# Optimization experiments

Hardware: AMD Instinct MI355X
Metric: run time of the kernel (lower is better)

Reference implementation:

```python
import jax, jax.numpy as jnp
import numpy as np

D_MODEL = 1024
N_HEAD = 16
D_K = D_MODEL // N_HEAD


def setup_inputs() -> dict:
    key = jax.random.key(0)
    ks = jax.random.split(key, 11)
    B, S = 2, 2048
    scale = 1.0 / np.sqrt(D_MODEL)
    inp = {
        "q": jax.random.normal(ks[0], (B, S, D_MODEL), jnp.float32),
        "k": jax.random.normal(ks[1], (B, S, D_MODEL), jnp.float32),
        "v": jax.random.normal(ks[2], (B, S, D_MODEL), jnp.float32),
        "Wq": jax.random.normal(ks[3], (D_MODEL, D_MODEL), jnp.float32) * scale,
        "bq": jnp.zeros((D_MODEL,), jnp.float32),
        "Wk": jax.random.normal(ks[4], (D_MODEL, D_MODEL), jnp.float32) * scale,
        "bk": jnp.zeros((D_MODEL,), jnp.float32),
        "Wv": jax.random.normal(ks[5], (D_MODEL, D_MODEL), jnp.float32) * scale,
        "bv": jnp.zeros((D_MODEL,), jnp.float32),
        "Wo": jax.random.normal(ks[6], (D_MODEL, D_MODEL), jnp.float32) * scale,
        "bo": jnp.zeros((D_MODEL,), jnp.float32),
    }
    return inp


def _split_heads(x):
    B, S, _ = x.shape
    return x.reshape(B, S, N_HEAD, D_K).transpose(0, 2, 1, 3)  # [B,H,S,Dk]


def reference(q, k, v, Wq, bq, Wk, bk, Wv, bv, Wo, bo):
    # Linear projections (torch Linear: x @ W.T + b)
    qh = _split_heads(q @ Wq.T + bq)
    kh = _split_heads(k @ Wk.T + bk)
    vh = _split_heads(v @ Wv.T + bv)
    # naive scaled dot-product attention, full [B,H,S,S] scores
    score = jnp.einsum("bhqd,bhkd->bhqk", qh, kh) / jnp.sqrt(jnp.float32(D_K))
    attn = jax.nn.softmax(score, axis=-1)
    out = jnp.einsum("bhqk,bhkd->bhqd", attn, vh)
    B, H, S, Dk = out.shape
    out = out.transpose(0, 2, 1, 3).reshape(B, S, H * Dk)
    return out @ Wo.T + bo
```

## Files before the change

kernel.cpp:

```cpp
#include <hip/hip_runtime.h>

typedef __attribute__((ext_vector_type(8))) short bh8;
typedef __attribute__((ext_vector_type(4))) float fx4;
typedef __attribute__((ext_vector_type(16))) float fx16;
typedef __attribute__((ext_vector_type(4))) unsigned short us4;
typedef unsigned short u16;

__device__ __forceinline__ u16 f2bf(float x) {
  unsigned u = __float_as_uint(x);
  u += 0x7fffu + ((u >> 16) & 1u);
  return (u16)(u >> 16);
}

__device__ __forceinline__ void async16(const void* g, void* l) {
  __builtin_amdgcn_global_load_lds(
      (const __attribute__((address_space(1))) void*)g,
      (__attribute__((address_space(3))) void*)l,
      16, 0, 0);
}

__global__ __launch_bounds__(256) void k_convert(
    const float* __restrict__ q, const float* __restrict__ k, const float* __restrict__ v,
    const float* __restrict__ wq, const float* __restrict__ wk,
    const float* __restrict__ wv, const float* __restrict__ wo,
    u16* __restrict__ dst) {
  size_t gid = (size_t)blockIdx.x * 256 + threadIdx.x;
  size_t e4 = gid * 4;
  const float* src; size_t off;
  if (e4 < 4194304)        { src = q;  off = e4; }
  else if (e4 < 8388608)   { src = k;  off = e4 - 4194304; }
  else if (e4 < 12582912)  { src = v;  off = e4 - 8388608; }
  else if (e4 < 13631488)  { src = wq; off = e4 - 12582912; }
  else if (e4 < 14680064)  { src = wk; off = e4 - 13631488; }
  else if (e4 < 15728640)  { src = wv; off = e4 - 14680064; }
  else                     { src = wo; off = e4 - 15728640; }
  float4 f = *(const float4*)(src + off);
  us4 o; o.x = f2bf(f.x); o.y = f2bf(f.y); o.z = f2bf(f.z); o.w = f2bf(f.w);
  *(us4*)(dst + e4) = o;
}

template<int BM>
__device__ __forceinline__ void gemm_stageT(const u16* __restrict__ A, const u16* __restrict__ B,
                                            char* lds, int bufbase, int m0, int n0, int kt, int tid) {
  int wb16 = (tid & 0xC0) * 16;
  #pragma unroll
  for (int i = 0; i < BM / 64; ++i) {
    int cl = i * 256 + tid;
    int row = cl >> 2, ch = cl & 3;
    int sch = ch ^ (row & 3);
    const char* ga = (const char*)(A + (size_t)(m0 + row) * 1024 + kt * 32) + sch * 16;
    async16(ga, lds + bufbase + i * 4096 + wb16);
  }
  #pragma unroll
  for (int i = 0; i < 2; ++i) {
    int cl = i * 256 + tid;
    int row = cl >> 2, ch = cl & 3;
    int sch = ch ^ (row & 3);
    const char* gb = (const char*)(B + (size_t)(n0 + row) * 1024 + kt * 32) + sch * 16;
    async16(gb, lds + bufbase + BM * 64 + i * 4096 + wb16);
  }
}

template<int BM>
__device__ __forceinline__ void gemm_coreT(const u16* __restrict__ A, const u16* __restrict__ Bw,
                                           const float* __restrict__ bias, void* Cout, int mode,
                                           float scl, char* lds) {
  constexpr int MF = BM / 32;
  constexpr int BUFSZ = BM * 64 + 8192;
  int tid = threadIdx.x;
  int lane = tid & 63, w = tid >> 6, g = lane >> 4, cc = lane & 15;
  int wr = w >> 1, wc = w & 1;
  int m0 = blockIdx.y * BM, n0 = blockIdx.x * 128;
  fx4 acc[MF][4] = {};
  gemm_stageT<BM>(A, Bw, lds, 0, m0, n0, 0, tid);
  for (int kt = 0; kt < 32; ++kt) {
    __syncthreads();
    if (kt + 1 < 32) gemm_stageT<BM>(A, Bw, lds, ((kt + 1) & 1) * BUFSZ, m0, n0, kt + 1, tid);
    const char* bA = lds + (kt & 1) * BUFSZ;
    const char* bB = bA + BM * 64;
    bh8 af[MF], bf[4];
    #pragma unroll
    for (int mf = 0; mf < MF; ++mf) {
      int row = wr * (BM / 2) + mf * 16 + cc;
      af[mf] = *(const bh8*)(bA + row * 64 + ((g ^ (row & 3)) * 16));
    }
    #pragma unroll
    for (int nf = 0; nf < 4; ++nf) {
      int row = wc * 64 + nf * 16 + cc;
      bf[nf] = *(const bh8*)(bB + row * 64 + ((g ^ (row & 3)) * 16));
    }
    #pragma unroll
    for (int mf = 0; mf < MF; ++mf)
      #pragma unroll
      for (int nf = 0; nf < 4; ++nf)
        acc[mf][nf] = __builtin_amdgcn_mfma_f32_16x16x32_bf16(af[mf], bf[nf], acc[mf][nf], 0, 0, 0);
  }
  #pragma unroll
  for (int mf = 0; mf < MF; ++mf) {
    #pragma unroll
    for (int nf = 0; nf < 4; ++nf) {
      fx4 a = acc[mf][nf];
      int row = m0 + wr * (BM / 2) + mf * 16 + g * 4;
      int col = n0 + wc * 64 + nf * 16 + cc;
      float bv = bias[col];
      if (mode == 0) {
        u16* C = (u16*)Cout;
        #pragma unroll
        for (int r = 0; r < 4; ++r) C[(size_t)(row + r) * 1024 + col] = f2bf((a[r] + bv) * scl);
      } else if (mode == 1) {
        float* C = (float*)Cout;
        #pragma unroll
        for (int r = 0; r < 4; ++r) C[(size_t)(row + r) * 1024 + col] = (a[r] + bv) * scl;
      } else {
        u16* C = (u16*)Cout;
        us4 o;
        #pragma unroll
        for (int r = 0; r < 4; ++r) o[r] = f2bf((a[r] + bv) * scl);
        int bb = row >> 11;
        *(us4*)(C + (size_t)(bb * 1024 + col) * 2048 + (row & 2047)) = o;
      }
    }
  }
}

__global__ __launch_bounds__(256) void k_gemm_qkv(
    const u16* __restrict__ qb, const u16* __restrict__ kb, const u16* __restrict__ vb,
    const u16* __restrict__ wqb, const u16* __restrict__ wkb, const u16* __restrict__ wvb,
    const float* __restrict__ bq, const float* __restrict__ bk, const float* __restrict__ bv,
    u16* __restrict__ Qp, u16* __restrict__ Kp, u16* __restrict__ Vt) {
  __shared__ __align__(16) char lds[32768];
  int z = blockIdx.z;
  const u16* A = (z == 0) ? qb : (z == 1) ? kb : vb;
  const u16* B = (z == 0) ? wqb : (z == 1) ? wkb : wvb;
  const float* bias = (z == 0) ? bq : (z == 1) ? bk : bv;
  void* C = (z == 0) ? (void*)Qp : (z == 1) ? (void*)Kp : (void*)Vt;
  float scl = (z == 0) ? 0.18033688f : 1.0f;
  gemm_coreT<128>(A, B, bias, C, (z == 2) ? 2 : 0, scl, lds);
}

__global__ __launch_bounds__(256) void k_gemm_out(
    const u16* __restrict__ Ob, const u16* __restrict__ wob,
    const float* __restrict__ bo, float* __restrict__ out) {
  __shared__ __align__(16) char lds[24576];
  gemm_coreT<64>(Ob, wob, bo, out, 1, 1.0f, lds);
}

__global__ __launch_bounds__(256) void k_attn(
    const u16* __restrict__ Qp, const u16* __restrict__ Kp,
    const u16* __restrict__ Vt, u16* __restrict__ O) {
  __shared__ __align__(16) char lds[65536];
  int tid = threadIdx.x;
  int lane = tid & 63, w = tid >> 6, ql = lane & 31, hi = lane >> 5;
  int lin = blockIdx.y * 16 + blockIdx.x;
  int xcd = lin & 7, slot = lin >> 3;
  int bh = xcd * 4 + (slot >> 4), qtile = slot & 15;
  int b = bh >> 4, h = bh & 15;
  int q0 = qtile * 128 + w * 32;
  size_t qrow = (size_t)b * 2048 + q0 + ql;
  bh8 qf[4];
  #pragma unroll
  for (int ds = 0; ds < 4; ++ds)
    qf[ds] = *(const bh8*)(Qp + qrow * 1024 + h * 64 + ds * 16 + hi * 8);

  int r0 = tid >> 3;
  int gr0 = (r0 & 19) | (((r0 >> 2) & 1) << 3) | (((r0 >> 3) & 1) << 2);
  int sK = (tid & 7) ^ (r0 & 7);
  const char* gK = (const char*)(Kp + (size_t)(b * 2048 + gr0) * 1024 + h * 64) + sK * 16;
  int vr0 = tid >> 4;
  int sV = (tid & 15) ^ (vr0 & 7);
  const char* gV = (const char*)(Vt + ((size_t)(b * 1024 + h * 64 + vr0)) * 2048) + sV * 16;
  int wb16 = (tid & 0xC0) * 16;

  int x7 = ql & 7;
  int kbase = ql * 128, vbase = ql * 256;
  int kc[4], vc[8];
  #pragma unroll
  for (int ds = 0; ds < 4; ++ds) kc[ds] = ((ds * 2 + hi) ^ x7) * 16;
  #pragma unroll
  for (int ks = 0; ks < 8; ++ks) vc[ks] = ((ks * 2 + hi) ^ x7) * 16;

  float lpart = 0.f;
  fx16 ot[2] = {};
  #pragma unroll
  for (int i = 0; i < 4; ++i) {
    async16(gK + i * 65536, lds + i * 4096 + wb16);
    async16(gV + i * 65536, lds + 16384 + i * 4096 + wb16);
  }
  gK += 262144; gV += 256;

  for (int t = 0; t < 16; ++t) {
    __syncthreads();
    if (t + 1 < 16) {
      int bb = ((t + 1) & 1) << 15;
      #pragma unroll
      for (int i = 0; i < 4; ++i) {
        async16(gK + i * 65536, lds + bb + i * 4096 + wb16);
        async16(gV + i * 65536, lds + bb + 16384 + i * 4096 + wb16);
      }
      gK += 262144; gV += 256;
    }
    const char* bK = lds + ((t & 1) << 15);
    const char* bV = bK + 16384;
    fx16 st[4] = {};
    #pragma unroll
    for (int kk = 0; kk < 4; ++kk)
      #pragma unroll
      for (int ds = 0; ds < 4; ++ds)
        st[kk] = __builtin_amdgcn_mfma_f32_32x32x16_bf16(
            *(const bh8*)(bK + kk * 4096 + kbase + kc[ds]), qf[ds], st[kk], 0, 0, 0);
    bh8 Pf[8];
    #pragma unroll
    for (int kk = 0; kk < 4; ++kk) {
      #pragma unroll
      for (int m = 0; m < 2; ++m) {
        float p[8];
        #pragma unroll
        for (int e = 0; e < 8; ++e) p[e] = __builtin_amdgcn_exp2f(st[kk][8 * m + e]);
        lpart += ((p[0] + p[1]) + (p[2] + p[3])) + ((p[4] + p[5]) + (p[6] + p[7]));
        unsigned u0, u1, u2, u3;
        asm("v_cvt_pk_bf16_f32 %0, %1, %2" : "=v"(u0) : "v"(p[0]), "v"(p[1]));
        asm("v_cvt_pk_bf16_f32 %0, %1, %2" : "=v"(u1) : "v"(p[2]), "v"(p[3]));
        asm("v_cvt_pk_bf16_f32 %0, %1, %2" : "=v"(u2) : "v"(p[4]), "v"(p[5]));
        asm("v_cvt_pk_bf16_f32 %0, %1, %2" : "=v"(u3) : "v"(p[6]), "v"(p[7]));
        union { unsigned u[4]; bh8 v; } pu;
        pu.u[0] = u0; pu.u[1] = u1; pu.u[2] = u2; pu.u[3] = u3;
        Pf[kk * 2 + m] = pu.v;
      }
    }
    #pragma unroll
    for (int dt = 0; dt < 2; ++dt)
      #pragma unroll
      for (int ks = 0; ks < 8; ++ks)
        ot[dt] = __builtin_amdgcn_mfma_f32_32x32x16_bf16(
            *(const bh8*)(bV + dt * 8192 + vbase + vc[ks]), Pf[ks], ot[dt], 0, 0, 0);
  }
  float lsum = lpart + __shfl_xor(lpart, 32);
  float inv = 1.f / lsum;
  #pragma unroll
  for (int dt = 0; dt < 2; ++dt)
    #pragma unroll
    for (int j = 0; j < 4; ++j) {
      us4 o4;
      #pragma unroll
      for (int i = 0; i < 4; ++i) o4[i] = f2bf(ot[dt][4 * j + i] * inv);
      *(us4*)(O + qrow * 1024 + h * 64 + dt * 32 + j * 8 + hi * 4) = o4;
    }
}

extern "C" void kernel_launch(void* const* d_in, const int* in_sizes, int n_in,
                              void* d_out, int out_size, void* d_ws, size_t ws_size,
                              hipStream_t stream) {
  const float* q  = (const float*)d_in[0];
  const float* k  = (const float*)d_in[1];
  const float* v  = (const float*)d_in[2];
  const float* Wq = (const float*)d_in[3];
  const float* bq = (const float*)d_in[4];
  const float* Wk = (const float*)d_in[5];
  const float* bk = (const float*)d_in[6];
  const float* Wv = (const float*)d_in[7];
  const float* bv = (const float*)d_in[8];
  const float* Wo = (const float*)d_in[9];
  const float* bo = (const float*)d_in[10];
  u16* ws  = (u16*)d_ws;
  u16* qb  = ws;
  u16* kb  = qb + 4194304;
  u16* vb  = kb + 4194304;
  u16* wqb = vb + 4194304;
  u16* wkb = wqb + 1048576;
  u16* wvb = wkb + 1048576;
  u16* wob = wvb + 1048576;
  u16* Qp  = wob + 1048576;
  u16* Kp  = Qp + 4194304;
  u16* Vt  = Kp + 4194304;
  u16* Ob  = qb;

  k_convert<<<dim3(16384), 256, 0, stream>>>(q, k, v, Wq, Wk, Wv, Wo, qb);
  k_gemm_qkv<<<dim3(8, 32, 3), 256, 0, stream>>>(qb, kb, vb, wqb, wkb, wvb, bq, bk, bv, Qp, Kp, Vt);
  k_attn<<<dim3(16, 32), 256, 0, stream>>>(Qp, Kp, Vt, Ob);
  k_gemm_out<<<dim3(8, 64), 256, 0, stream>>>(Ob, wob, bo, (float*)d_out);
}
```

Measured before the change: 122.8 us.

## Fuse fp32-to-bf16 activation conversion into QKV GEMM A-tile staging

The separate conversion pass over q, k and v is removed; the QKV GEMM now loads fp32 activation tiles into registers, converts them with packed bf16 conversion instructions and writes them into swizzled LDS. The register loads for the next tile are issued before the MFMA loop and stored after it, to overlap them with compute. This avoids writing and re-reading 24M bf16 activation elements, at the cost of reading fp32 A from global memory once per N-tile column (eight times) and moving A staging off the async global-to-LDS path. The rounding mode may differ slightly from the previous manual round-to-nearest-even.

```diff
diff --git a/kernel.cpp b/kernel.cpp
--- a/kernel.cpp
+++ b/kernel.cpp
@@ -20,28 +20,38 @@
 }
 
 __global__ __launch_bounds__(256) void k_convert(
-    const float* __restrict__ q, const float* __restrict__ k, const float* __restrict__ v,
     const float* __restrict__ wq, const float* __restrict__ wk,
     const float* __restrict__ wv, const float* __restrict__ wo,
     u16* __restrict__ dst) {
   size_t gid = (size_t)blockIdx.x * 256 + threadIdx.x;
   size_t e4 = gid * 4;
   const float* src; size_t off;
-  if (e4 < 4194304)        { src = q;  off = e4; }
-  else if (e4 < 8388608)   { src = k;  off = e4 - 4194304; }
-  else if (e4 < 12582912)  { src = v;  off = e4 - 8388608; }
-  else if (e4 < 13631488)  { src = wq; off = e4 - 12582912; }
-  else if (e4 < 14680064)  { src = wk; off = e4 - 13631488; }
-  else if (e4 < 15728640)  { src = wv; off = e4 - 14680064; }
-  else                     { src = wo; off = e4 - 15728640; }
+  if (e4 < 1048576)        { src = wq; off = e4; }
+  else if (e4 < 2097152)   { src = wk; off = e4 - 1048576; }
+  else if (e4 < 3145728)   { src = wv; off = e4 - 2097152; }
+  else                     { src = wo; off = e4 - 3145728; }
   float4 f = *(const float4*)(src + off);
   us4 o; o.x = f2bf(f.x); o.y = f2bf(f.y); o.z = f2bf(f.z); o.w = f2bf(f.w);
   *(us4*)(dst + e4) = o;
 }
 
 template<int BM>
-__device__ __forceinline__ void gemm_stageT(const u16* __restrict__ A, const u16* __restrict__ B,
-                                            char* lds, int bufbase, int m0, int n0, int kt, int tid) {
+__device__ __forceinline__ void gemm_stageB(const u16* __restrict__ B, char* lds, int bufbase,
+                                            int n0, int kt, int tid) {
+  int wb16 = (tid & 0xC0) * 16;
+  #pragma unroll
+  for (int i = 0; i < 2; ++i) {
+    int cl = i * 256 + tid;
+    int row = cl >> 2, ch = cl & 3;
+    int sch = ch ^ (row & 3);
+    const char* gb = (const char*)(B + (size_t)(n0 + row) * 1024 + kt * 32) + sch * 16;
+    async16(gb, lds + bufbase + BM * 64 + i * 4096 + wb16);
+  }
+}
+
+template<int BM>
+__device__ __forceinline__ void gemm_stageA16(const u16* __restrict__ A, char* lds, int bufbase,
+                                              int m0, int kt, int tid) {
   int wb16 = (tid & 0xC0) * 16;
   #pragma unroll
   for (int i = 0; i < BM / 64; ++i) {
@@ -51,31 +61,61 @@
     const char* ga = (const char*)(A + (size_t)(m0 + row) * 1024 + kt * 32) + sch * 16;
     async16(ga, lds + bufbase + i * 4096 + wb16);
   }
-  #pragma unroll
-  for (int i = 0; i < 2; ++i) {
-    int cl = i * 256 + tid;
-    int row = cl >> 2, ch = cl & 3;
-    int sch = ch ^ (row & 3);
-    const char* gb = (const char*)(B + (size_t)(n0 + row) * 1024 + kt * 32) + sch * 16;
-    async16(gb, lds + bufbase + BM * 64 + i * 4096 + wb16);
-  }
-}
-
-template<int BM>
-__device__ __forceinline__ void gemm_coreT(const u16* __restrict__ A, const u16* __restrict__ Bw,
+}
+
+__device__ __forceinline__ void cvt_write16(char* dst, float4 lo, float4 hi) {
+  unsigned u0, u1, u2, u3;
+  asm("v_cvt_pk_bf16_f32 %0, %1, %2" : "=v"(u0) : "v"(lo.x), "v"(lo.y));
+  asm("v_cvt_pk_bf16_f32 %0, %1, %2" : "=v"(u1) : "v"(lo.z), "v"(lo.w));
+  asm("v_cvt_pk_bf16_f32 %0, %1, %2" : "=v"(u2) : "v"(hi.x), "v"(hi.y));
+  asm("v_cvt_pk_bf16_f32 %0, %1, %2" : "=v"(u3) : "v"(hi.z), "v"(hi.w));
+  union { unsigned u[4]; bh8 v; } pu;
+  pu.u[0] = u0; pu.u[1] = u1; pu.u[2] = u2; pu.u[3] = u3;
+  *(bh8*)dst = pu.v;
+}
+
+template<int BM, bool AF32>
+__device__ __forceinline__ void gemm_coreT(const void* __restrict__ Ain, const u16* __restrict__ Bw,
                                            const float* __restrict__ bias, void* Cout, int mode,
                                            float scl, char* lds) {
   constexpr int MF = BM / 32;
   constexpr int BUFSZ = BM * 64 + 8192;
+  const float* A32 = (const float*)Ain;
+  const u16*   A16 = (const u16*)Ain;
   int tid = threadIdx.x;
   int lane = tid & 63, w = tid >> 6, g = lane >> 4, cc = lane & 15;
   int wr = w >> 1, wc = w & 1;
   int m0 = blockIdx.y * BM, n0 = blockIdx.x * 128;
+  int srow = tid >> 2, sch0 = tid & 3;
+  int adst = srow * 64 + ((sch0 ^ (srow & 3)) * 16);
   fx4 acc[MF][4] = {};
-  gemm_stageT<BM>(A, Bw, lds, 0, m0, n0, 0, tid);
+  if constexpr (AF32) {
+    #pragma unroll
+    for (int i = 0; i < BM / 64; ++i) {
+      const float* s = A32 + (size_t)(m0 + srow + i * 64) * 1024 + sch0 * 8;
+      cvt_write16(lds + i * 4096 + adst, *(const float4*)s, *(const float4*)(s + 4));
+    }
+  } else {
+    gemm_stageA16<BM>(A16, lds, 0, m0, 0, tid);
+  }
+  gemm_stageB<BM>(Bw, lds, 0, n0, 0, tid);
   for (int kt = 0; kt < 32; ++kt) {
     __syncthreads();
-    if (kt + 1 < 32) gemm_stageT<BM>(A, Bw, lds, ((kt + 1) & 1) * BUFSZ, m0, n0, kt + 1, tid);
+    int bufn = ((kt + 1) & 1) * BUFSZ;
+    float4 la[BM / 64][2];
+    if (kt + 1 < 32) {
+      if constexpr (AF32) {
+        #pragma unroll
+        for (int i = 0; i < BM / 64; ++i) {
+          const float* s = A32 + (size_t)(m0 + srow + i * 64) * 1024 + (kt + 1) * 32 + sch0 * 8;
+          la[i][0] = *(const float4*)s;
+          la[i][1] = *(const float4*)(s + 4);
+        }
+      } else {
+        gemm_stageA16<BM>(A16, lds, bufn, m0, kt + 1, tid);
+      }
+      gemm_stageB<BM>(Bw, lds, bufn, n0, kt + 1, tid);
+    }
     const char* bA = lds + (kt & 1) * BUFSZ;
     const char* bB = bA + BM * 64;
     bh8 af[MF], bf[4];
@@ -94,6 +134,13 @@
       #pragma unroll
       for (int nf = 0; nf < 4; ++nf)
         acc[mf][nf] = __builtin_amdgcn_mfma_f32_16x16x32_bf16(af[mf], bf[nf], acc[mf][nf], 0, 0, 0);
+    if constexpr (AF32) {
+      if (kt + 1 < 32) {
+        #pragma unroll
+        for (int i = 0; i < BM / 64; ++i)
+          cvt_write16(lds + bufn + i * 4096 + adst, la[i][0], la[i][1]);
+      }
+    }
   }
   #pragma unroll
   for (int mf = 0; mf < MF; ++mf) {
@@ -124,25 +171,25 @@
 }
 
 __global__ __launch_bounds__(256) void k_gemm_qkv(
-    const u16* __restrict__ qb, const u16* __restrict__ kb, const u16* __restrict__ vb,
+    const float* __restrict__ q, const float* __restrict__ k, const float* __restrict__ v,
     const u16* __restrict__ wqb, const u16* __restrict__ wkb, const u16* __restrict__ wvb,
     const float* __restrict__ bq, const float* __restrict__ bk, const float* __restrict__ bv,
     u16* __restrict__ Qp, u16* __restrict__ Kp, u16* __restrict__ Vt) {
   __shared__ __align__(16) char lds[32768];
   int z = blockIdx.z;
-  const u16* A = (z == 0) ? qb : (z == 1) ? kb : vb;
+  const float* A = (z == 0) ? q : (z == 1) ? k : v;
   const u16* B = (z == 0) ? wqb : (z == 1) ? wkb : wvb;
   const float* bias = (z == 0) ? bq : (z == 1) ? bk : bv;
   void* C = (z == 0) ? (void*)Qp : (z == 1) ? (void*)Kp : (void*)Vt;
   float scl = (z == 0) ? 0.18033688f : 1.0f;
-  gemm_coreT<128>(A, B, bias, C, (z == 2) ? 2 : 0, scl, lds);
+  gemm_coreT<128, true>(A, B, bias, C, (z == 2) ? 2 : 0, scl, lds);
 }
 
 __global__ __launch_bounds__(256) void k_gemm_out(
     const u16* __restrict__ Ob, const u16* __restrict__ wob,
     const float* __restrict__ bo, float* __restrict__ out) {
   __shared__ __align__(16) char lds[24576];
-  gemm_coreT<64>(Ob, wob, bo, out, 1, 1.0f, lds);
+  gemm_coreT<64, false>(Ob, wob, bo, out, 1, 1.0f, lds);
 }
 
 __global__ __launch_bounds__(256) void k_attn(
@@ -274,8 +321,8 @@
   u16* Vt  = Kp + 4194304;
   u16* Ob  = qb;
 
-  k_convert<<<dim3(16384), 256, 0, stream>>>(q, k, v, Wq, Wk, Wv, Wo, qb);
-  k_gemm_qkv<<<dim3(8, 32, 3), 256, 0, stream>>>(qb, kb, vb, wqb, wkb, wvb, bq, bk, bv, Qp, Kp, Vt);
+  k_convert<<<dim3(4096), 256, 0, stream>>>(Wq, Wk, Wv, Wo, wqb);
+  k_gemm_qkv<<<dim3(8, 32, 3), 256, 0, stream>>>(q, k, v, wqb, wkb, wvb, bq, bk, bv, Qp, Kp, Vt);
   k_attn<<<dim3(16, 32), 256, 0, stream>>>(Qp, Kp, Vt, Ob);
   k_gemm_out<<<dim3(8, 64), 256, 0, stream>>>(Ob, wob, bo, (float*)d_out);
 }
```

Result: slower. 133.0 us (+8.4%).
